# Performance work log

Measured on AMD Instinct MI355X. Metric: run time of the kernel, lower is better.

Reference implementation:

```python
import jax, jax.numpy as jnp
import numpy as np

D_K = 64  # hardcoded in source module

def setup_inputs() -> dict:
    key = jax.random.key(0)
    kq, kk, kv, km = jax.random.split(key, 4)
    B, H, S, D = 2, 16, 2048, D_K
    Q = jax.random.normal(kq, (B, H, S, D), dtype=jnp.float32)
    K = jax.random.normal(kk, (B, H, S, D), dtype=jnp.float32)
    V = jax.random.normal(kv, (B, H, S, D), dtype=jnp.float32)
    # boolean mask: True positions are masked out (filled with -1e9)
    attn_mask = jax.random.randint(km, (B, H, S, S), 0, 2) == 1
    return {"Q": Q, "K": K, "V": V, "attn_mask": attn_mask}

def reference(Q, K, V, attn_mask):
    scale = 1.0 / np.sqrt(D_K).astype(np.float32)
    # scores: [B, H, S, S]
    scores = jnp.einsum('bhqd,bhkd->bhqk', Q, K) * scale
    scores = jnp.where(attn_mask, jnp.float32(-1e9), scores)
    attn = jax.nn.softmax(scores, axis=-1)
    context = jnp.einsum('bhqk,bhkd->bhqd', attn, V)
    return context
```

## Files before the change

kernel.cpp:

```cpp
#include <hip/hip_runtime.h>

#define SEQ   2048
#define DK    64
#define QBLK  64
#define KVBLK 64
#define NTILE (SEQ / KVBLK)
#define PITCH 72

typedef __attribute__((ext_vector_type(8))) __bf16 bf16x8;
typedef __attribute__((ext_vector_type(4))) __bf16 bf16x4;
typedef __attribute__((ext_vector_type(4))) float  f32x4;
typedef __attribute__((ext_vector_type(4))) int    i32x4;

__device__ __forceinline__ float grp16_max(float v) {
  v = fmaxf(v, __shfl_xor(v, 1));
  v = fmaxf(v, __shfl_xor(v, 2));
  v = fmaxf(v, __shfl_xor(v, 4));
  v = fmaxf(v, __shfl_xor(v, 8));
  return v;
}
__device__ __forceinline__ float grp16_sum(float v) {
  v += __shfl_xor(v, 1);
  v += __shfl_xor(v, 2);
  v += __shfl_xor(v, 4);
  v += __shfl_xor(v, 8);
  return v;
}

__global__ __launch_bounds__(256, 2)
void sdpa_fwd(const float* __restrict__ Q, const float* __restrict__ K,
              const float* __restrict__ V, const int* __restrict__ M,
              float* __restrict__ O)
{
  __shared__ __bf16 Klds[KVBLK][PITCH];
  __shared__ __bf16 Vt[DK][PITCH];
  __shared__ __bf16 Plds[4][16][PITCH];

  const int tid  = threadIdx.x;
  const int w    = tid >> 6;
  const int lane = tid & 63;
  const int g    = lane >> 4;
  const int li   = lane & 15;

  const int blk = blockIdx.x;
  const int qb  = blk & (SEQ / QBLK - 1);
  const int bh  = blk >> 5;

  const float* Qp = Q + (size_t)bh * SEQ * DK;
  const float* Kp = K + (size_t)bh * SEQ * DK;
  const float* Vp = V + (size_t)bh * SEQ * DK;
  const int*   Mp = M + (size_t)bh * SEQ * SEQ;
  float*       Op = O + (size_t)bh * SEQ * DK;

  const int q0 = qb * QBLK + w * 16;

  const int sk = tid >> 2;
  const int sd = (tid & 3) * 16;
  const int sj = ((sk & 3) << 4) | (sk >> 2);

  bf16x8 qfrag[2];
  {
    const float qs = 0.125f * 1.44269504088896340736f;
    const float* qr = Qp + (size_t)(q0 + li) * DK + g * 8;
    #pragma unroll
    for (int h2 = 0; h2 < 2; ++h2) {
      f32x4 a = *(const f32x4*)(qr + h2 * 32);
      f32x4 b = *(const f32x4*)(qr + h2 * 32 + 4);
      bf16x8 f;
      #pragma unroll
      for (int e = 0; e < 4; ++e) {
        f[e]     = (__bf16)(a[e] * qs);
        f[4 + e] = (__bf16)(b[e] * qs);
      }
      qfrag[h2] = f;
    }
  }

  f32x4 acc[4];
  #pragma unroll
  for (int c = 0; c < 4; ++c) acc[c] = (f32x4){0.f, 0.f, 0.f, 0.f};
  float m_r[4], l_r[4];
  #pragma unroll
  for (int r = 0; r < 4; ++r) { m_r[r] = -__builtin_inff(); l_r[r] = 0.f; }

  f32x4 kA[4], vA[4];
  i32x4 mA[4];

  {
    const float* ks = Kp + (size_t)sk * DK + sd;
    const float* vs = Vp + (size_t)sk * DK + sd;
    #pragma unroll
    for (int i = 0; i < 4; ++i) { kA[i] = *(const f32x4*)(ks + 4 * i); vA[i] = *(const f32x4*)(vs + 4 * i); }
    #pragma unroll
    for (int r = 0; r < 4; ++r)
      mA[r] = *(const i32x4*)(Mp + (size_t)(q0 + 4 * g + r) * SEQ + li * 4);
  }

  for (int kt = 0; kt < NTILE; ++kt) {
    __syncthreads();

    {
      bf16x8 klo, khi;
      #pragma unroll
      for (int e = 0; e < 4; ++e) {
        klo[e]     = (__bf16)kA[0][e];
        klo[4 + e] = (__bf16)kA[1][e];
        khi[e]     = (__bf16)kA[2][e];
        khi[4 + e] = (__bf16)kA[3][e];
      }
      *(bf16x8*)&Klds[sj][sd]     = klo;
      *(bf16x8*)&Klds[sj][sd + 8] = khi;
      #pragma unroll
      for (int qd = 0; qd < 4; ++qd)
        #pragma unroll
        for (int e = 0; e < 4; ++e)
          Vt[sd + qd * 4 + e][sk] = (__bf16)vA[qd][e];
    }

    i32x4 msk[4];
    #pragma unroll
    for (int r = 0; r < 4; ++r) msk[r] = mA[r];

    if (kt + 1 < NTILE) {
      const int kvn = (kt + 1) * KVBLK;
      const float* ks = Kp + (size_t)(kvn + sk) * DK + sd;
      const float* vs = Vp + (size_t)(kvn + sk) * DK + sd;
      #pragma unroll
      for (int i = 0; i < 4; ++i) { kA[i] = *(const f32x4*)(ks + 4 * i); vA[i] = *(const f32x4*)(vs + 4 * i); }
      #pragma unroll
      for (int r = 0; r < 4; ++r)
        mA[r] = *(const i32x4*)(Mp + (size_t)(q0 + 4 * g + r) * SEQ + kvn + li * 4);
    }

    __syncthreads();

    f32x4 st[4];
    #pragma unroll
    for (int nt = 0; nt < 4; ++nt) {
      bf16x8 b0 = *(const bf16x8*)&Klds[nt * 16 + li][g * 8];
      bf16x8 b1 = *(const bf16x8*)&Klds[nt * 16 + li][32 + g * 8];
      f32x4 s = (f32x4){0.f, 0.f, 0.f, 0.f};
      s = __builtin_amdgcn_mfma_f32_16x16x32_bf16(qfrag[0], b0, s, 0, 0, 0);
      s = __builtin_amdgcn_mfma_f32_16x16x32_bf16(qfrag[1], b1, s, 0, 0, 0);
      st[nt] = s;
    }

    #pragma unroll
    for (int r = 0; r < 4; ++r) {
      float s0 = msk[r].x ? -1e9f : st[0][r];
      float s1 = msk[r].y ? -1e9f : st[1][r];
      float s2 = msk[r].z ? -1e9f : st[2][r];
      float s3 = msk[r].w ? -1e9f : st[3][r];
      float mx    = grp16_max(fmaxf(fmaxf(s0, s1), fmaxf(s2, s3)));
      float mnew  = fmaxf(m_r[r], mx);
      float alpha = __builtin_amdgcn_exp2f(m_r[r] - mnew);
      float p0 = __builtin_amdgcn_exp2f(s0 - mnew);
      float p1 = __builtin_amdgcn_exp2f(s1 - mnew);
      float p2 = __builtin_amdgcn_exp2f(s2 - mnew);
      float p3 = __builtin_amdgcn_exp2f(s3 - mnew);
      l_r[r] = l_r[r] * alpha + grp16_sum((p0 + p1) + (p2 + p3));
      m_r[r] = mnew;
      acc[0][r] *= alpha;
      acc[1][r] *= alpha;
      acc[2][r] *= alpha;
      acc[3][r] *= alpha;
      bf16x4 pk;
      pk[0] = (__bf16)p0; pk[1] = (__bf16)p1; pk[2] = (__bf16)p2; pk[3] = (__bf16)p3;
      *(bf16x4*)&Plds[w][4 * g + r][li * 4] = pk;
    }

    asm volatile("s_waitcnt lgkmcnt(0)" ::: "memory");
    __builtin_amdgcn_sched_barrier(0);

    bf16x8 pa0 = *(const bf16x8*)&Plds[w][li][g * 8];
    bf16x8 pa1 = *(const bf16x8*)&Plds[w][li][32 + g * 8];
    #pragma unroll
    for (int dt = 0; dt < 4; ++dt) {
      bf16x8 v0 = *(const bf16x8*)&Vt[dt * 16 + li][g * 8];
      bf16x8 v1 = *(const bf16x8*)&Vt[dt * 16 + li][32 + g * 8];
      acc[dt] = __builtin_amdgcn_mfma_f32_16x16x32_bf16(pa0, v0, acc[dt], 0, 0, 0);
      acc[dt] = __builtin_amdgcn_mfma_f32_16x16x32_bf16(pa1, v1, acc[dt], 0, 0, 0);
    }
  }

  #pragma unroll
  for (int r = 0; r < 4; ++r) {
    float inv = 1.0f / l_r[r];
    float* orow = Op + (size_t)(q0 + 4 * g + r) * DK + li;
    #pragma unroll
    for (int dt = 0; dt < 4; ++dt)
      orow[dt * 16] = acc[dt][r] * inv;
  }
}

extern "C" void kernel_launch(void* const* d_in, const int* in_sizes, int n_in,
                              void* d_out, int out_size, void* d_ws, size_t ws_size,
                              hipStream_t stream) {
  const float* Q = (const float*)d_in[0];
  const float* K = (const float*)d_in[1];
  const float* V = (const float*)d_in[2];
  const int*   M = (const int*)d_in[3];
  float*       O = (float*)d_out;

  const int nblocks = 2 * 16 * (SEQ / QBLK);
  sdpa_fwd<<<nblocks, 256, 0, stream>>>(Q, K, V, M, O);
}
```

Measured before the change: 753.9 us.

## Prefetch mask two tiles ahead, use LDS-only barriers, swizzle block order

The mask loads are now issued two KV tiles ahead, using two register sets swapped across a manually unrolled loop body. The last tiles wrap around and load tile 0 redundantly instead of branching. __syncthreads is replaced by a barrier that waits only on LDS counters, so outstanding global loads are not drained at each sync. Block IDs are remapped so that consecutive blocks spread across heads, which may change L2/XCD locality. The cost is more registers for the mask prefetch and extra memory traffic from the wrapped loads.

```diff
diff --git a/kernel.cpp b/kernel.cpp
--- a/kernel.cpp
+++ b/kernel.cpp
@@ -26,6 +26,18 @@
   v += __shfl_xor(v, 8);
   return v;
 }
+
+__device__ __forceinline__ void block_sync_lds() {
+  asm volatile("s_waitcnt lgkmcnt(0)" ::: "memory");
+  __builtin_amdgcn_sched_barrier(0);
+  __builtin_amdgcn_s_barrier();
+  __builtin_amdgcn_sched_barrier(0);
+}
+
+struct KState {
+  const float* Kp; const float* Vp; const int* Mp;
+  int sk, sd, sj, g, li, w, q0;
+};
 
 __global__ __launch_bounds__(256, 2)
 void sdpa_fwd(const float* __restrict__ Q, const float* __restrict__ K,
@@ -42,7 +54,8 @@
   const int g    = lane >> 4;
   const int li   = lane & 15;
 
-  const int blk = blockIdx.x;
+  const int bid = blockIdx.x;
+  const int blk = (bid & 7) * 128 + (bid >> 3);
   const int qb  = blk & (SEQ / QBLK - 1);
   const int bh  = blk >> 5;
 
@@ -68,10 +81,7 @@
       f32x4 b = *(const f32x4*)(qr + h2 * 32 + 4);
       bf16x8 f;
       #pragma unroll
-      for (int e = 0; e < 4; ++e) {
-        f[e]     = (__bf16)(a[e] * qs);
-        f[4 + e] = (__bf16)(b[e] * qs);
-      }
+      for (int e = 0; e < 4; ++e) { f[e] = (__bf16)(a[e] * qs); f[4 + e] = (__bf16)(b[e] * qs); }
       qfrag[h2] = f;
     }
   }
@@ -84,7 +94,7 @@
   for (int r = 0; r < 4; ++r) { m_r[r] = -__builtin_inff(); l_r[r] = 0.f; }
 
   f32x4 kA[4], vA[4];
-  i32x4 mA[4];
+  i32x4 mA[4], mB[4];
 
   {
     const float* ks = Kp + (size_t)sk * DK + sd;
@@ -92,21 +102,22 @@
     #pragma unroll
     for (int i = 0; i < 4; ++i) { kA[i] = *(const f32x4*)(ks + 4 * i); vA[i] = *(const f32x4*)(vs + 4 * i); }
     #pragma unroll
-    for (int r = 0; r < 4; ++r)
-      mA[r] = *(const i32x4*)(Mp + (size_t)(q0 + 4 * g + r) * SEQ + li * 4);
-  }
-
-  for (int kt = 0; kt < NTILE; ++kt) {
-    __syncthreads();
+    for (int r = 0; r < 4; ++r) {
+      const size_t mrow = (size_t)(q0 + 4 * g + r) * SEQ + li * 4;
+      mA[r] = *(const i32x4*)(Mp + mrow);
+      mB[r] = *(const i32x4*)(Mp + mrow + KVBLK);
+    }
+  }
+
+  auto body = [&](int kt, i32x4 (&mc)[4], i32x4 (&mn)[4]) {
+    block_sync_lds();
 
     {
       bf16x8 klo, khi;
       #pragma unroll
       for (int e = 0; e < 4; ++e) {
-        klo[e]     = (__bf16)kA[0][e];
-        klo[4 + e] = (__bf16)kA[1][e];
-        khi[e]     = (__bf16)kA[2][e];
-        khi[4 + e] = (__bf16)kA[3][e];
+        klo[e] = (__bf16)kA[0][e]; klo[4 + e] = (__bf16)kA[1][e];
+        khi[e] = (__bf16)kA[2][e]; khi[4 + e] = (__bf16)kA[3][e];
       }
       *(bf16x8*)&Klds[sj][sd]     = klo;
       *(bf16x8*)&Klds[sj][sd + 8] = khi;
@@ -119,20 +130,21 @@
 
     i32x4 msk[4];
     #pragma unroll
-    for (int r = 0; r < 4; ++r) msk[r] = mA[r];
-
-    if (kt + 1 < NTILE) {
-      const int kvn = (kt + 1) * KVBLK;
-      const float* ks = Kp + (size_t)(kvn + sk) * DK + sd;
-      const float* vs = Vp + (size_t)(kvn + sk) * DK + sd;
+    for (int r = 0; r < 4; ++r) msk[r] = mc[r];
+
+    {
+      const int tm = (kt + 2 < NTILE) ? kt + 2 : 0;
+      #pragma unroll
+      for (int r = 0; r < 4; ++r)
+        mc[r] = *(const i32x4*)(Mp + (size_t)(q0 + 4 * g + r) * SEQ + tm * KVBLK + li * 4);
+      const int tn = (kt + 1 < NTILE) ? kt + 1 : 0;
+      const float* ks = Kp + (size_t)(tn * KVBLK + sk) * DK + sd;
+      const float* vs = Vp + (size_t)(tn * KVBLK + sk) * DK + sd;
       #pragma unroll
       for (int i = 0; i < 4; ++i) { kA[i] = *(const f32x4*)(ks + 4 * i); vA[i] = *(const f32x4*)(vs + 4 * i); }
-      #pragma unroll
-      for (int r = 0; r < 4; ++r)
-        mA[r] = *(const i32x4*)(Mp + (size_t)(q0 + 4 * g + r) * SEQ + kvn + li * 4);
-    }
-
-    __syncthreads();
+    }
+
+    block_sync_lds();
 
     f32x4 st[4];
     #pragma unroll
@@ -181,6 +193,11 @@
       acc[dt] = __builtin_amdgcn_mfma_f32_16x16x32_bf16(pa0, v0, acc[dt], 0, 0, 0);
       acc[dt] = __builtin_amdgcn_mfma_f32_16x16x32_bf16(pa1, v1, acc[dt], 0, 0, 0);
     }
+  };
+
+  for (int kt = 0; kt < NTILE; kt += 2) {
+    body(kt, mA, mB);
+    body(kt + 1, mB, mA);
   }
 
   #pragma unroll
```

Measured after the change: 768.2 us. About the same (+1.9%).
